# Kernel optimization log

Measured on AMD Instinct MI355X. Metric: run time of the kernel, lower is better.

## Reference

```python
import jax, jax.numpy as jnp
import numpy as np

FP8_MAX = 448.0  # float8_e4m3fn max (use_e4m3=True)
K, N = 512, 512


def setup_inputs() -> dict:
    key = jax.random.key(0)
    kx, kw = jax.random.split(key)
    x = jax.random.normal(kx, (8, 8192, K), dtype=jnp.float32)
    weight = jax.random.normal(kw, (K, N), dtype=jnp.float32) * 0.02
    return {"x": x, "weight": weight}


def reference(x, weight):
    B, S, _ = x.shape
    x2d = x.reshape(-1, K)  # [M, K]

    # dynamic per-tensor quantization of activations to fp8 e4m3
    x_amax = jnp.max(jnp.abs(x2d))
    x_scale = FP8_MAX / jnp.maximum(x_amax, 1e-12)
    x_fp8 = jnp.clip(x2d * x_scale, -FP8_MAX, FP8_MAX).astype(jnp.float8_e4m3fn)

    # dynamic per-tensor quantization of weight (transposed, as in source)
    w_amax = jnp.max(jnp.abs(weight))
    w_scale = FP8_MAX / jnp.maximum(w_amax, 1e-12)
    w_fp8 = jnp.clip(weight.T * w_scale, -FP8_MAX, FP8_MAX).astype(jnp.float8_e4m3fn)  # [N, K]

    # cast-up matmul then dequantize with combined inverse scale
    res = jnp.matmul(x_fp8.astype(jnp.float32), w_fp8.astype(jnp.float32).T)  # [M, N]
    out = res * ((1.0 / x_scale) * (1.0 / w_scale))
    return out.reshape(B, S, N).astype(x.dtype)
```

## Files before the change

kernel.cpp:

```cpp
#include <hip/hip_runtime.h>

typedef float f32x4 __attribute__((ext_vector_type(4)));
typedef long i64;

#define KDIM 512
#define NDIM 512
#define LDS_STRIDE 520
#define OUT_STRIDE 260

__device__ __forceinline__ float clamp448(float v) {
    return fminf(fmaxf(v, -448.0f), 448.0f);
}

__global__ __launch_bounds__(256) void amax_kernel(const float4* __restrict__ x,
                                                   const float4* __restrict__ w,
                                                   unsigned* __restrict__ scales) {
    const int tid = threadIdx.x;
    float m = 0.0f;
    if (blockIdx.x < 4096) {
        int base = blockIdx.x * 256 + tid;
        #pragma unroll
        for (int j = 0; j < 8; ++j) {
            float4 v = x[base + j * 1048576];
            m = fmaxf(m, fmaxf(fmaxf(fabsf(v.x), fabsf(v.y)), fmaxf(fabsf(v.z), fabsf(v.w))));
        }
    } else {
        int base = (blockIdx.x - 4096) * 256 + tid;
        #pragma unroll
        for (int j = 0; j < 8; ++j) {
            float4 v = w[base + j * 8192];
            m = fmaxf(m, fmaxf(fmaxf(fabsf(v.x), fabsf(v.y)), fmaxf(fabsf(v.z), fabsf(v.w))));
        }
    }
    #pragma unroll
    for (int off = 32; off > 0; off >>= 1)
        m = fmaxf(m, __shfl_down(m, off, 64));
    __shared__ float red[4];
    const int wave = tid >> 6, lane = tid & 63;
    if (lane == 0) red[wave] = m;
    __syncthreads();
    if (tid == 0) {
        m = fmaxf(fmaxf(red[0], red[1]), fmaxf(red[2], red[3]));
        atomicMax(&scales[blockIdx.x < 4096 ? 0 : 1], __float_as_uint(m));
    }
}

__global__ __launch_bounds__(256) void wquant_kernel(const float4* __restrict__ wv,
                                                     const unsigned* __restrict__ scales,
                                                     unsigned char* __restrict__ wq) {
    const float ws = 448.0f / fmaxf(__uint_as_float(scales[1]), 1e-12f);
    #pragma unroll
    for (int j = 0; j < 4; ++j) {
        const int idx = blockIdx.x * 1024 + j * 256 + threadIdx.x;
        const int k = idx >> 7;
        const int n4 = idx & 127;
        float4 v = wv[idx];
        float a[4] = {v.x, v.y, v.z, v.w};
        #pragma unroll
        for (int i = 0; i < 4; ++i) {
            float q = clamp448(a[i] * ws);
            int p = __builtin_amdgcn_cvt_pk_fp8_f32(q, q, 0, false);
            wq[(n4 * 4 + i) * KDIM + k] = (unsigned char)(p & 0xff);
        }
    }
}

__global__ __launch_bounds__(256, 4) void gemm_kernel(const float* __restrict__ x,
                                                      const unsigned char* __restrict__ wq,
                                                      const unsigned* __restrict__ scales,
                                                      float* __restrict__ out) {
    __shared__ unsigned char lds_a[64 * LDS_STRIDE];
    __shared__ float lds_o[16 * OUT_STRIDE];
    const int tid = threadIdx.x;
    const long m0 = (long)blockIdx.x * 64;

    const float ax = fmaxf(__uint_as_float(scales[0]), 1e-12f);
    const float aw = fmaxf(__uint_as_float(scales[1]), 1e-12f);
    const float xs = 448.0f / ax;
    const float ws = 448.0f / aw;
    const float inv = (1.0f / xs) * (1.0f / ws);

    const float4* xv = (const float4*)(x + m0 * KDIM);
    #pragma unroll 8
    for (int j = 0; j < 32; ++j) {
        int f4i = tid + 256 * j;
        float4 v = xv[f4i];
        int row = f4i >> 7;
        int colb = (f4i & 127) << 2;
        float a0 = clamp448(v.x * xs);
        float a1 = clamp448(v.y * xs);
        float a2 = clamp448(v.z * xs);
        float a3 = clamp448(v.w * xs);
        int p = __builtin_amdgcn_cvt_pk_fp8_f32(a0, a1, 0, false);
        p = __builtin_amdgcn_cvt_pk_fp8_f32(a2, a3, p, true);
        *(unsigned*)&lds_a[row * LDS_STRIDE + colb] = (unsigned)p;
    }
    __syncthreads();

    const int wave = tid >> 6, lane = tid & 63;
    const int ln = lane & 15, lg = lane >> 4;
    const int kofs = lg * 8;
    float* outp = out + m0 * NDIM;

    for (int chunk = 0; chunk < 2; ++chunk) {
        const int nbase = chunk * 256 + wave * 64;
        f32x4 acc[4][4];
        #pragma unroll
        for (int a = 0; a < 4; ++a)
            #pragma unroll
            for (int b = 0; b < 4; ++b)
                acc[a][b] = (f32x4){0.0f, 0.0f, 0.0f, 0.0f};

        for (int ks = 0; ks < 16; ++ks) {
            const int kb = ks * 32 + kofs;
            i64 af[4], bf[4];
            #pragma unroll
            for (int t = 0; t < 4; ++t)
                af[t] = *(const i64*)&lds_a[(t * 16 + ln) * LDS_STRIDE + kb];
            #pragma unroll
            for (int t = 0; t < 4; ++t)
                bf[t] = *(const i64*)&wq[(nbase + t * 16 + ln) * KDIM + kb];
            #pragma unroll
            for (int tm = 0; tm < 4; ++tm)
                #pragma unroll
                for (int tn = 0; tn < 4; ++tn)
                    acc[tm][tn] = __builtin_amdgcn_mfma_f32_16x16x32_fp8_fp8(
                        af[tm], bf[tn], acc[tm][tn], 0, 0, 0);
        }

        #pragma unroll 1
        for (int tm = 0; tm < 4; ++tm) {
            __syncthreads();
            #pragma unroll
            for (int tn = 0; tn < 4; ++tn) {
                const int c = wave * 64 + tn * 16 + ln;
                #pragma unroll
                for (int r = 0; r < 4; ++r)
                    lds_o[(lg * 4 + r) * OUT_STRIDE + c] = acc[tm][tn][r] * inv;
            }
            __syncthreads();
            #pragma unroll
            for (int j = 0; j < 4; ++j) {
                const int idx = j * 256 + tid;
                const int rr = idx >> 6;
                const int c4 = idx & 63;
                float4 v = *(const float4*)&lds_o[rr * OUT_STRIDE + c4 * 4];
                *(float4*)&outp[(long)(tm * 16 + rr) * NDIM + chunk * 256 + c4 * 4] = v;
            }
        }
    }
}

extern "C" void kernel_launch(void* const* d_in, const int* in_sizes, int n_in,
                              void* d_out, int out_size, void* d_ws, size_t ws_size,
                              hipStream_t stream) {
    const float* x = (const float*)d_in[0];
    const float* w = (const float*)d_in[1];
    float* out = (float*)d_out;
    unsigned* scales = (unsigned*)d_ws;
    unsigned char* wq = (unsigned char*)d_ws + 256;
    const int M = in_sizes[0] / KDIM;

    hipMemsetAsync(d_ws, 0, 8, stream);
    amax_kernel<<<4096 + 32, 256, 0, stream>>>((const float4*)x, (const float4*)w, scales);
    wquant_kernel<<<64, 256, 0, stream>>>((const float4*)w, scales, wq);
    gemm_kernel<<<M / 64, 256, 0, stream>>>(x, wq, scales, out);
}
```

Measured before the change: 355.5 us.

## Replace atomic amax with two-pass reduction and write GEMM output directly

The per-block atomicMax plus memset is replaced by per-block partial maxima written to workspace, followed by a single-block reduce kernel. The GEMM epilogue no longer stages output through LDS with barriers; each lane stores its accumulator values straight to global memory. This drops the barriers and the LDS footprint in the epilogue, which may help occupancy, but the direct stores are scalar, strided 4-byte writes and less coalesced than the float4 row writes they replace. It also adds one more kernel launch.

```diff
diff --git a/kernel.cpp b/kernel.cpp
--- a/kernel.cpp
+++ b/kernel.cpp
@@ -6,7 +6,6 @@
 #define KDIM 512
 #define NDIM 512
 #define LDS_STRIDE 520
-#define OUT_STRIDE 260
 
 __device__ __forceinline__ float clamp448(float v) {
     return fminf(fmaxf(v, -448.0f), 448.0f);
@@ -14,7 +13,7 @@
 
 __global__ __launch_bounds__(256) void amax_kernel(const float4* __restrict__ x,
                                                    const float4* __restrict__ w,
-                                                   unsigned* __restrict__ scales) {
+                                                   float* __restrict__ partial) {
     const int tid = threadIdx.x;
     float m = 0.0f;
     if (blockIdx.x < 4096) {
@@ -39,16 +38,37 @@
     const int wave = tid >> 6, lane = tid & 63;
     if (lane == 0) red[wave] = m;
     __syncthreads();
+    if (tid == 0)
+        partial[blockIdx.x] = fmaxf(fmaxf(red[0], red[1]), fmaxf(red[2], red[3]));
+}
+
+__global__ __launch_bounds__(256) void reduce_kernel(const float* __restrict__ partial,
+                                                     float* __restrict__ scales) {
+    const int tid = threadIdx.x;
+    float mx = 0.0f, mw = 0.0f;
+    #pragma unroll
+    for (int j = 0; j < 16; ++j)
+        mx = fmaxf(mx, partial[j * 256 + tid]);
+    if (tid < 32) mw = partial[4096 + tid];
+    #pragma unroll
+    for (int off = 32; off > 0; off >>= 1) {
+        mx = fmaxf(mx, __shfl_down(mx, off, 64));
+        mw = fmaxf(mw, __shfl_down(mw, off, 64));
+    }
+    __shared__ float red[8];
+    const int wave = tid >> 6, lane = tid & 63;
+    if (lane == 0) { red[wave] = mx; red[4 + wave] = mw; }
+    __syncthreads();
     if (tid == 0) {
-        m = fmaxf(fmaxf(red[0], red[1]), fmaxf(red[2], red[3]));
-        atomicMax(&scales[blockIdx.x < 4096 ? 0 : 1], __float_as_uint(m));
+        scales[0] = fmaxf(fmaxf(red[0], red[1]), fmaxf(red[2], red[3]));
+        scales[1] = fmaxf(fmaxf(red[4], red[5]), fmaxf(red[6], red[7]));
     }
 }
 
 __global__ __launch_bounds__(256) void wquant_kernel(const float4* __restrict__ wv,
-                                                     const unsigned* __restrict__ scales,
+                                                     const float* __restrict__ scales,
                                                      unsigned char* __restrict__ wq) {
-    const float ws = 448.0f / fmaxf(__uint_as_float(scales[1]), 1e-12f);
+    const float ws = 448.0f / fmaxf(scales[1], 1e-12f);
     #pragma unroll
     for (int j = 0; j < 4; ++j) {
         const int idx = blockIdx.x * 1024 + j * 256 + threadIdx.x;
@@ -67,15 +87,14 @@
 
 __global__ __launch_bounds__(256, 4) void gemm_kernel(const float* __restrict__ x,
                                                       const unsigned char* __restrict__ wq,
-                                                      const unsigned* __restrict__ scales,
+                                                      const float* __restrict__ scales,
                                                       float* __restrict__ out) {
     __shared__ unsigned char lds_a[64 * LDS_STRIDE];
-    __shared__ float lds_o[16 * OUT_STRIDE];
     const int tid = threadIdx.x;
     const long m0 = (long)blockIdx.x * 64;
 
-    const float ax = fmaxf(__uint_as_float(scales[0]), 1e-12f);
-    const float aw = fmaxf(__uint_as_float(scales[1]), 1e-12f);
+    const float ax = fmaxf(scales[0], 1e-12f);
+    const float aw = fmaxf(scales[1], 1e-12f);
     const float xs = 448.0f / ax;
     const float ws = 448.0f / aw;
     const float inv = (1.0f / xs) * (1.0f / ws);
@@ -128,24 +147,14 @@
                         af[tm], bf[tn], acc[tm][tn], 0, 0, 0);
         }
 
-        #pragma unroll 1
+        #pragma unroll
         for (int tm = 0; tm < 4; ++tm) {
-            __syncthreads();
             #pragma unroll
             for (int tn = 0; tn < 4; ++tn) {
-                const int c = wave * 64 + tn * 16 + ln;
+                const int c = nbase + tn * 16 + ln;
                 #pragma unroll
                 for (int r = 0; r < 4; ++r)
-                    lds_o[(lg * 4 + r) * OUT_STRIDE + c] = acc[tm][tn][r] * inv;
-            }
-            __syncthreads();
-            #pragma unroll
-            for (int j = 0; j < 4; ++j) {
-                const int idx = j * 256 + tid;
-                const int rr = idx >> 6;
-                const int c4 = idx & 63;
-                float4 v = *(const float4*)&lds_o[rr * OUT_STRIDE + c4 * 4];
-                *(float4*)&outp[(long)(tm * 16 + rr) * NDIM + chunk * 256 + c4 * 4] = v;
+                    outp[(long)(tm * 16 + lg * 4 + r) * NDIM + c] = acc[tm][tn][r] * inv;
             }
         }
     }
@@ -157,12 +166,13 @@
     const float* x = (const float*)d_in[0];
     const float* w = (const float*)d_in[1];
     float* out = (float*)d_out;
-    unsigned* scales = (unsigned*)d_ws;
+    float* scales = (float*)d_ws;
     unsigned char* wq = (unsigned char*)d_ws + 256;
+    float* partial = (float*)((char*)d_ws + 256 + 262144);
     const int M = in_sizes[0] / KDIM;
 
-    hipMemsetAsync(d_ws, 0, 8, stream);
-    amax_kernel<<<4096 + 32, 256, 0, stream>>>((const float4*)x, (const float4*)w, scales);
+    amax_kernel<<<4096 + 32, 256, 0, stream>>>((const float4*)x, (const float4*)w, partial);
+    reduce_kernel<<<1, 256, 0, stream>>>(partial, scales);
     wquant_kernel<<<64, 256, 0, stream>>>((const float4*)w, scales, wq);
     gemm_kernel<<<M / 64, 256, 0, stream>>>(x, wq, scales, out);
 }
```

Result: slower. 389.1 us (+9.4%).
